# Kernel tuning notes

Measured on AMD Instinct MI355X. Metric: run time of the kernel, lower is better.

## Reference

```python
import jax, jax.numpy as jnp
import numpy as np

GC_ALPHA = 3.0  # saturation factor in MTGNN-style graph constructor
TOP_K = 5       # ctor arg: GraphConstructor(n_classes, 5, dim)
EPS_NORM = 1e-12


def setup_inputs() -> dict:
    key = jax.random.key(0)
    k1, k2, k3, k4, k5 = jax.random.split(key, 5)
    B, C, H, W = 32, 384, 80, 80
    N = 27
    return {
        "x": jax.random.normal(k1, (B, C, H, W), dtype=jnp.float32),
        "alpha": jnp.ones((), dtype=jnp.float32),
        "clusters": jax.random.normal(k2, (N, C), dtype=jnp.float32),
        "gc_w1": jax.random.normal(k3, (C, C), dtype=jnp.float32) / np.sqrt(C),
        "gc_w2": jax.random.normal(k4, (C, C), dtype=jnp.float32) / np.sqrt(C),
        "gcn_w": jax.random.normal(k5, (C, C), dtype=jnp.float32) / np.sqrt(C),
    }


def _refine_clusters(clusters, gc_w1, gc_w2, gcn_w):
    # GraphConstructor: learned asymmetric adjacency over n_classes nodes, top-k sparsified
    n = clusters.shape[0]
    a = jnp.tanh(GC_ALPHA * (clusters @ gc_w1))          # [n, d]
    b = jnp.tanh(GC_ALPHA * (clusters @ gc_w2))          # [n, d]
    adj = jax.nn.relu(jnp.tanh(GC_ALPHA * (a @ b.T - b @ a.T)))  # [n, n]
    topv, _ = jax.lax.top_k(adj, TOP_K)
    A = jnp.where(adj >= topv[:, -1:], adj, 0.0)         # keep top-k per row
    # GCNConv (no bias): add self-loops, symmetric normalization
    A_hat = A + jnp.eye(n, dtype=A.dtype)
    dinv = 1.0 / jnp.sqrt(A_hat.sum(axis=1))
    A_norm = dinv[:, None] * A_hat * dinv[None, :]
    return A_norm @ (clusters @ gcn_w)                   # [n, d]


def reference(x, alpha, clusters, gc_w1, gc_w2, gcn_w):
    # mp=True path: refine codebook with tiny GCN over learned graph
    cl = _refine_clusters(clusters, gc_w1, gc_w2, gcn_w)
    # cosine similarity of per-pixel features against codebook
    nc = cl / jnp.maximum(jnp.linalg.norm(cl, axis=1, keepdims=True), EPS_NORM)
    nf = x / jnp.maximum(jnp.linalg.norm(x, axis=1, keepdims=True), EPS_NORM)
    inner_products = jnp.einsum('bchw,nc->bnhw', nf, nc)          # [B, n, H, W]
    cluster_probs = jax.nn.softmax(inner_products * alpha, axis=1)
    cluster_loss = -(cluster_probs * inner_products).sum(axis=1).mean()
    # entropy over unnormalized similarities (computed in original forward)
    p = jax.nn.softmax(jnp.einsum('bchw,nc->bnhw', x, clusters), axis=1)
    entropy = (-(p * jnp.log(p + 1e-10)).sum(axis=1)).mean()
    return cluster_loss, inner_products, cl, entropy
```

## Files before the change

### kernel.cpp

```cpp
#include <hip/hip_runtime.h>
#include <math.h>

#define N_CL   27
#define C_DIM  384
#define HW_SZ  6400
#define B_SZ   32
#define NPIX   (B_SZ*HW_SZ)
#define NTILE  3200
#define NCHUNK 12
#define WSF_PARTS 24576
#define WSF_ADJ   40000
#define ENT_OFF (1 + (size_t)NPIX*N_CL + (size_t)N_CL*C_DIM)

typedef unsigned short ushort_t;
using bf16x8 = __attribute__((ext_vector_type(8))) short;
using f32x4  = __attribute__((ext_vector_type(4))) float;

__device__ __forceinline__ float xla_tanh_f32(float x) {
    const float c = 7.99881172180175781f;
    if (fabsf(x) < 0.0004f) return x;
    const float xc = fminf(fmaxf(x, -c), c);
    const float x2 = xc*xc;
    float p = fmaf(x2, -2.76076847742355e-16f, 2.00018790482477e-13f);
    p = fmaf(x2, p, -8.60467152213735e-11f);
    p = fmaf(x2, p,  5.12229709037114e-08f);
    p = fmaf(x2, p,  1.48572235717979e-05f);
    p = fmaf(x2, p,  6.37261928875436e-04f);
    p = fmaf(x2, p,  4.89352455891786e-03f);
    p = xc*p;
    float q = fmaf(x2, 1.19825839466702e-06f, 1.18534705686654e-04f);
    q = fmaf(x2, q, 2.26843463243900e-03f);
    q = fmaf(x2, q, 4.89352518554385e-03f);
    return p/q;
}

__global__ __launch_bounds__(384) void cl_refine_mm(const float* __restrict__ clusters,
                                                    const float* __restrict__ w1,
                                                    const float* __restrict__ w2,
                                                    const float* __restrict__ w3,
                                                    float* __restrict__ ws) {
    const int i = blockIdx.x;
    const int m = blockIdx.y;
    const int j = threadIdx.x;
    __shared__ float crow[C_DIM];
    crow[j] = clusters[i*C_DIM + j];
    __syncthreads();
    const float* __restrict__ W = (m==0) ? w1 : (m==1) ? w2 : w3;
    float s0=0.f,s1=0.f,s2=0.f,s3=0.f;
    #pragma unroll 4
    for (int k=0;k<C_DIM;k+=4){
        s0 = fmaf(crow[k+0], W[(size_t)(k+0)*C_DIM + j], s0);
        s1 = fmaf(crow[k+1], W[(size_t)(k+1)*C_DIM + j], s1);
        s2 = fmaf(crow[k+2], W[(size_t)(k+2)*C_DIM + j], s2);
        s3 = fmaf(crow[k+3], W[(size_t)(k+3)*C_DIM + j], s3);
    }
    const float acc = (s0+s1)+(s2+s3);
    ws[(size_t)m*N_CL*C_DIM + i*C_DIM + j] = (m<2) ? xla_tanh_f32(3.0f*acc) : acc;
}

__global__ __launch_bounds__(64) void cl_adj(const float* __restrict__ ws,
                                             float* __restrict__ adj_out) {
    const float* __restrict__ Am = ws;
    const float* __restrict__ Bm = ws + N_CL*C_DIM;
    const int i = blockIdx.x / N_CL, j = blockIdx.x - (blockIdx.x / N_CL)*N_CL;
    const int lane = threadIdx.x;
    float p=0.f, q=0.f;
    #pragma unroll
    for (int e=0;e<6;e++){
        const int k = e*64 + lane;
        p = fmaf(Am[i*C_DIM+k], Bm[j*C_DIM+k], p);
        q = fmaf(Bm[i*C_DIM+k], Am[j*C_DIM+k], q);
    }
    float d = p - q;
    #pragma unroll
    for (int m=1;m<64;m<<=1) d += __shfl_xor(d, m);
    if (lane==0) adj_out[blockIdx.x] = fmaxf(xla_tanh_f32(3.0f*d), 0.f);
}

__global__ __launch_bounds__(1024) void cl_graph2(float* ws,
                                                  const float* __restrict__ clusters_g,
                                                  float* __restrict__ out) {
    const float* cg = ws + 2*N_CL*C_DIM;
    float* cl_out = out + 1 + (size_t)NPIX*N_CL;
    const int t = threadIdx.x;

    __shared__ float anorm[N_CL][N_CL+1];
    __shared__ float dinv[N_CL];
    __shared__ float rinv[N_CL];
    __shared__ float cls[N_CL][C_DIM];

    if (t < N_CL*N_CL) {
        const int i = t / N_CL, j = t - (t / N_CL)*N_CL;
        anorm[i][j] = ws[WSF_ADJ + t];
    }
    __syncthreads();
    if (t < N_CL) {
        unsigned mask=0; float thr=0.f;
        for (int s=0;s<5;s++){
            float bv=-1.f; int bi2=0;
            for (int j=0;j<N_CL;j++){
                if (mask & (1u<<j)) continue;
                const float v = anorm[t][j];
                if (v > bv){ bv=v; bi2=j; }
            }
            mask |= 1u<<bi2; thr = bv;
        }
        float rs=0.f;
        for (int j=0;j<N_CL;j++){
            float v = anorm[t][j];
            v = (v >= thr) ? v : 0.f;
            if (j==t) v += 1.f;
            anorm[t][j] = v;
            rs += v;
        }
        dinv[t] = 1.0f / sqrtf(rs);
    }
    __syncthreads();
    if (t < N_CL*N_CL) {
        const int i = t / N_CL, j = t - (t / N_CL)*N_CL;
        anorm[i][j] = dinv[i]*anorm[i][j]*dinv[j];
    }
    __syncthreads();
    for (int idx=t; idx<N_CL*C_DIM; idx+=1024){
        const int i = idx / C_DIM, d = idx - i*C_DIM;
        float s=0.f;
        #pragma unroll
        for (int j=0;j<N_CL;j++) s = fmaf(anorm[i][j], cg[(size_t)j*C_DIM + d], s);
        cls[i][d] = s;
        cl_out[idx] = s;
    }
    __syncthreads();
    if (t < N_CL) {
        float ssq=0.f;
        for (int d=0; d<C_DIM; d++){ const float v=cls[t][d]; ssq=fmaf(v,v,ssq); }
        rinv[t] = 1.0f / fmaxf(sqrtf(ssq), 1e-12f);
    }
    __syncthreads();
    ushort_t* wpk = (ushort_t*)ws;
    for (int idx=t; idx<64*C_DIM; idx+=1024){
        const int n = idx / C_DIM, k = idx - n*C_DIM;
        float v = 0.f;
        if (n < N_CL) v = cls[n][k] * rinv[n];
        else if (n >= 32 && n < 32+N_CL) v = clusters_g[(size_t)(n-32)*C_DIM + k];
        const unsigned bits = __float_as_uint(v);
        const ushort_t hi = (ushort_t)(bits >> 16);
        const float lof = v - __uint_as_float(bits & 0xFFFF0000u);
        const ushort_t lo = (ushort_t)(__float_as_uint(lof) >> 16);
        wpk[idx] = hi;
        wpk[64*C_DIM + idx] = lo;
    }
}

__global__ __launch_bounds__(256, 6) void cl_mfma(const float* __restrict__ x,
                                                  const float* __restrict__ alpha_p,
                                                  const ushort_t* __restrict__ wpk,
                                                  float* __restrict__ ws,
                                                  float* __restrict__ out) {
    __shared__ __align__(16) ushort_t lB[2][2][64][40];
    __shared__ float redL[4], redE[4];

    const int tid = threadIdx.x;
    const int blk = blockIdx.x;
    const int b   = blk / 100;
    const int hw0 = (blk - b*100) * 64;
    const float* __restrict__ xb = x + (size_t)b*C_DIM*HW_SZ + hw0;

    const int lane = tid & 63;
    const int w    = tid >> 6;
    const int l15  = lane & 15;
    const int g    = lane >> 4;
    const int k0   = g*8;
    const int apx  = w*16 + l15;
    const float* __restrict__ xl = xb + apx;

    const int b_n  = tid >> 2;
    const int b_kb = (tid & 3) * 8;

    uint4 rb0, rb1;
    #define LOADB(c) {                                                            \
        rb0 = *(const uint4*)(wpk + (size_t)(     b_n)*C_DIM + (c)*32 + b_kb);    \
        rb1 = *(const uint4*)(wpk + (size_t)(64 + b_n)*C_DIM + (c)*32 + b_kb); }
    #define WRITEB(bf) {                                                          \
        *(uint4*)(&lB[bf][0][b_n][b_kb]) = rb0;                                   \
        *(uint4*)(&lB[bf][1][b_n][b_kb]) = rb1; }

    #define LOADA(c, R0,R1,R2,R3,R4,R5,R6,R7) {                                   \
        const float* pA = xl + (size_t)((c)*32 + k0)*HW_SZ;                       \
        R0 = pA[0*HW_SZ]; R1 = pA[1*HW_SZ]; R2 = pA[2*HW_SZ]; R3 = pA[3*HW_SZ];  \
        R4 = pA[4*HW_SZ]; R5 = pA[5*HW_SZ]; R6 = pA[6*HW_SZ]; R7 = pA[7*HW_SZ]; }

    union { ushort_t u[8]; bf16x8 v; } Ah;
    float ss = 0.f;
    #define CVT1(e, R) {                                                          \
        Ah.u[e] = (ushort_t)(__float_as_uint(R) >> 16);                           \
        ss = fmaf(R, R, ss); }
    #define CONVERT(R0,R1,R2,R3,R4,R5,R6,R7) {                                    \
        CVT1(0,R0) CVT1(1,R1) CVT1(2,R2) CVT1(3,R3)                               \
        CVT1(4,R4) CVT1(5,R5) CVT1(6,R6) CVT1(7,R7) }

    f32x4 acc0={0,0,0,0}, acc1={0,0,0,0}, acc2={0,0,0,0}, acc3={0,0,0,0};
    #define DOMFMA(cur) {                                                         \
        _Pragma("unroll")                                                         \
        for (int t = 0; t < 4; t++) {                                             \
            union { uint4 q; bf16x8 v; } Bh, Bl;                                  \
            Bh.q = *(const uint4*)(&lB[cur][0][t*16 + l15][k0]);                  \
            Bl.q = *(const uint4*)(&lB[cur][1][t*16 + l15][k0]);                  \
            f32x4 a = (t==0)?acc0:(t==1)?acc1:(t==2)?acc2:acc3;                   \
            a = __builtin_amdgcn_mfma_f32_16x16x32_bf16(Ah.v, Bh.v, a, 0,0,0);    \
            a = __builtin_amdgcn_mfma_f32_16x16x32_bf16(Ah.v, Bl.v, a, 0,0,0);    \
            if (t==0) acc0=a; else if (t==1) acc1=a; else if (t==2) acc2=a;       \
            else acc3=a;                                                          \
        } }

    #define KBAR() { asm volatile("s_waitcnt lgkmcnt(0)" ::: "memory");           \
                     __builtin_amdgcn_s_barrier(); }

    float Ra0,Ra1,Ra2,Ra3,Ra4,Ra5,Ra6,Ra7;
    float Rb0,Rb1,Rb2,Rb3,Rb4,Rb5,Rb6,Rb7;

    LOADB(0); WRITEB(0);
    LOADB(1);
    LOADA(0, Ra0,Ra1,Ra2,Ra3,Ra4,Ra5,Ra6,Ra7);
    LOADA(1, Rb0,Rb1,Rb2,Rb3,Rb4,Rb5,Rb6,Rb7);
    KBAR();

    for (int cc = 0; cc < NCHUNK; cc += 2) {
        CONVERT(Ra0,Ra1,Ra2,Ra3,Ra4,Ra5,Ra6,Ra7);
        DOMFMA(0);
        if (cc + 1 < NCHUNK) WRITEB(1);
        if (cc + 2 < NCHUNK) {
            LOADB(cc+2);
            LOADA(cc+2, Ra0,Ra1,Ra2,Ra3,Ra4,Ra5,Ra6,Ra7);
        }
        if (cc + 1 < NCHUNK) KBAR();
        CONVERT(Rb0,Rb1,Rb2,Rb3,Rb4,Rb5,Rb6,Rb7);
        DOMFMA(1);
        if (cc + 2 < NCHUNK) WRITEB(0);
        if (cc + 3 < NCHUNK) {
            LOADB(cc+3);
            LOADA(cc+3, Rb0,Rb1,Rb2,Rb3,Rb4,Rb5,Rb6,Rb7);
        }
        if (cc + 2 < NCHUNK) KBAR();
    }

    ss += __shfl_xor(ss, 16);
    ss += __shfl_xor(ss, 32);
    f32x4 invv;
    #pragma unroll
    for (int r = 0; r < 4; r++) {
        const float s2 = __shfl(ss, g*4 + r);
        invv[r] = 1.0f / fmaxf(sqrtf(s2), 1e-12f);
    }

    const float alpha = alpha_p[0];
    float* __restrict__ out1 = out + 1;
    const int pxb = hw0 + w*16 + g*4;

    f32x4 st0, st1;
    #pragma unroll
    for (int r=0;r<4;r++){ st0[r] = acc0[r]*invv[r]; st1[r] = acc1[r]*invv[r]; }
    *(f32x4*)(out1 + (size_t)b*N_CL*HW_SZ + (size_t)l15*HW_SZ + pxb) = st0;
    if (l15 <= 10)
        *(f32x4*)(out1 + (size_t)b*N_CL*HW_SZ + (size_t)(16+l15)*HW_SZ + pxb) = st1;

    float wloss = 0.f, went = 0.f;
    #pragma unroll
    for (int r=0;r<4;r++){
        const float ip0 = st0[r], ip1 = st1[r];
        const float v0 = alpha*ip0;
        const float v1 = (l15<=10) ? alpha*ip1 : -INFINITY;
        float mx = fmaxf(v0, v1);
        #pragma unroll
        for (int m=1;m<16;m<<=1) mx = fmaxf(mx, __shfl_xor(mx, m));
        const float e0 = expf(v0 - mx);
        const float e1 = (l15<=10) ? expf(v1 - mx) : 0.f;
        float z = e0 + e1;
        float tt = fmaf(e0, ip0, (l15<=10) ? e1*ip1 : 0.f);
        #pragma unroll
        for (int m=1;m<16;m<<=1){ z += __shfl_xor(z,m); tt += __shfl_xor(tt,m); }
        wloss += tt/z;
        const float c0 = acc2[r];
        const float c1 = (l15<=10) ? acc3[r] : -INFINITY;
        float emx = fmaxf(c0, c1);
        #pragma unroll
        for (int m=1;m<16;m<<=1) emx = fmaxf(emx, __shfl_xor(emx, m));
        const float f0 = expf(c0 - emx);
        const float f1 = (l15<=10) ? expf(c1 - emx) : 0.f;
        float ez = f0 + f1;
        #pragma unroll
        for (int m=1;m<16;m<<=1) ez += __shfl_xor(ez,m);
        const float iz = 1.0f/ez;
        const float p0 = f0*iz, p1 = f1*iz;
        float te = -p0*logf(p0+1e-10f) - p1*logf(p1+1e-10f);
        #pragma unroll
        for (int m=1;m<16;m<<=1) te += __shfl_xor(te,m);
        went += te;
    }
    wloss += __shfl_xor(wloss,16); wloss += __shfl_xor(wloss,32);
    went  += __shfl_xor(went ,16); went  += __shfl_xor(went ,32);
    if (lane == 0) { redL[w] = wloss; redE[w] = went; }
    __syncthreads();
    if (tid == 0) {
        float* parts = ws + WSF_PARTS;
        parts[blk]         = redL[0]+redL[1]+redL[2]+redL[3];
        parts[NTILE + blk] = redE[0]+redE[1]+redE[2]+redE[3];
    }
}

__global__ __launch_bounds__(1024) void cl_final_reduce(const float* __restrict__ ws,
                                                        float* __restrict__ out) {
    __shared__ float r[1024];
    const int t = threadIdx.x;
    const float* parts = ws + WSF_PARTS;
    float s = 0.f;
    for (int j=t; j<NTILE; j+=1024) s += parts[j];
    r[t] = s; __syncthreads();
    for (int sft=512;sft>0;sft>>=1){ if (t<sft) r[t]+=r[t+sft]; __syncthreads(); }
    if (t==0) out[0] = -r[0]*(1.0f/NPIX);
    __syncthreads();
    s = 0.f;
    for (int j=t; j<NTILE; j+=1024) s += parts[NTILE + j];
    r[t] = s; __syncthreads();
    for (int sft=512;sft>0;sft>>=1){ if (t<sft) r[t]+=r[t+sft]; __syncthreads(); }
    if (t==0) out[ENT_OFF] = r[0]*(1.0f/NPIX);
}

extern "C" void kernel_launch(void* const* d_in, const int* in_sizes, int n_in,
                              void* d_out, int out_size, void* d_ws, size_t ws_size,
                              hipStream_t stream) {
    const float* x        = (const float*)d_in[0];
    const float* alpha    = (const float*)d_in[1];
    const float* clusters = (const float*)d_in[2];
    const float* w1       = (const float*)d_in[3];
    const float* w2       = (const float*)d_in[4];
    const float* w3       = (const float*)d_in[5];
    float* out = (float*)d_out;
    float* ws  = (float*)d_ws;

    cl_refine_mm<<<dim3(27,3), dim3(384), 0, stream>>>(clusters, w1, w2, w3, ws);
    cl_adj<<<dim3(N_CL*N_CL), dim3(64), 0, stream>>>(ws, ws + WSF_ADJ);
    cl_graph2<<<dim3(1), dim3(1024), 0, stream>>>(ws, clusters, out);
    cl_mfma<<<dim3(NTILE), dim3(256), 0, stream>>>(x, alpha, (const ushort_t*)ws, ws, out);
    cl_final_reduce<<<dim3(1), dim3(1024), 0, stream>>>(ws, out);
}
```

Baseline: 140.3 us.

## Fuse adjacency into graph kernel and final reduce into main kernel via ticket

```diff
diff --git a/kernel.cpp b/kernel.cpp
--- a/kernel.cpp
+++ b/kernel.cpp
@@ -9,7 +9,7 @@
 #define NTILE  3200
 #define NCHUNK 12
 #define WSF_PARTS 24576
-#define WSF_ADJ   40000
+#define WSF_CNT   31104
 #define ENT_OFF (1 + (size_t)NPIX*N_CL + (size_t)N_CL*C_DIM)
 
 typedef unsigned short ushort_t;
@@ -58,40 +58,37 @@
     ws[(size_t)m*N_CL*C_DIM + i*C_DIM + j] = (m<2) ? xla_tanh_f32(3.0f*acc) : acc;
 }
 
-__global__ __launch_bounds__(64) void cl_adj(const float* __restrict__ ws,
-                                             float* __restrict__ adj_out) {
-    const float* __restrict__ Am = ws;
-    const float* __restrict__ Bm = ws + N_CL*C_DIM;
-    const int i = blockIdx.x / N_CL, j = blockIdx.x - (blockIdx.x / N_CL)*N_CL;
-    const int lane = threadIdx.x;
-    float p=0.f, q=0.f;
-    #pragma unroll
-    for (int e=0;e<6;e++){
-        const int k = e*64 + lane;
-        p = fmaf(Am[i*C_DIM+k], Bm[j*C_DIM+k], p);
-        q = fmaf(Bm[i*C_DIM+k], Am[j*C_DIM+k], q);
-    }
-    float d = p - q;
-    #pragma unroll
-    for (int m=1;m<64;m<<=1) d += __shfl_xor(d, m);
-    if (lane==0) adj_out[blockIdx.x] = fmaxf(xla_tanh_f32(3.0f*d), 0.f);
-}
-
-__global__ __launch_bounds__(1024) void cl_graph2(float* ws,
-                                                  const float* __restrict__ clusters_g,
-                                                  float* __restrict__ out) {
+__global__ __launch_bounds__(1024) void cl_adj_graph(float* ws,
+                                                     const float* __restrict__ clusters_g,
+                                                     float* __restrict__ out) {
     const float* cg = ws + 2*N_CL*C_DIM;
     float* cl_out = out + 1 + (size_t)NPIX*N_CL;
     const int t = threadIdx.x;
 
+    __shared__ float Ash[N_CL][C_DIM+1];
+    __shared__ float Bsh[N_CL][C_DIM+1];
     __shared__ float anorm[N_CL][N_CL+1];
     __shared__ float dinv[N_CL];
     __shared__ float rinv[N_CL];
     __shared__ float cls[N_CL][C_DIM];
 
+    for (int idx=t; idx<N_CL*C_DIM; idx+=1024){
+        const int i = idx / C_DIM, k = idx - i*C_DIM;
+        Ash[i][k] = ws[idx];
+        Bsh[i][k] = ws[N_CL*C_DIM + idx];
+    }
+    __syncthreads();
     if (t < N_CL*N_CL) {
         const int i = t / N_CL, j = t - (t / N_CL)*N_CL;
-        anorm[i][j] = ws[WSF_ADJ + t];
+        float p0=0,p1=0,p2=0,p3=0,q0=0,q1=0,q2=0,q3=0;
+        for (int k=0;k<C_DIM;k+=4){
+            p0=fmaf(Ash[i][k+0],Bsh[j][k+0],p0); p1=fmaf(Ash[i][k+1],Bsh[j][k+1],p1);
+            p2=fmaf(Ash[i][k+2],Bsh[j][k+2],p2); p3=fmaf(Ash[i][k+3],Bsh[j][k+3],p3);
+            q0=fmaf(Bsh[i][k+0],Ash[j][k+0],q0); q1=fmaf(Bsh[i][k+1],Ash[j][k+1],q1);
+            q2=fmaf(Bsh[i][k+2],Ash[j][k+2],q2); q3=fmaf(Bsh[i][k+3],Ash[j][k+3],q3);
+        }
+        const float s1v=(p0+p1)+(p2+p3), s2v=(q0+q1)+(q2+q3);
+        anorm[i][j] = fmaxf(xla_tanh_f32(3.0f*(s1v-s2v)), 0.f);
     }
     __syncthreads();
     if (t < N_CL) {
@@ -135,6 +132,7 @@
         for (int d=0; d<C_DIM; d++){ const float v=cls[t][d]; ssq=fmaf(v,v,ssq); }
         rinv[t] = 1.0f / fmaxf(sqrtf(ssq), 1e-12f);
     }
+    if (t == 0) *(unsigned*)(ws + WSF_CNT) = 0u;
     __syncthreads();
     ushort_t* wpk = (ushort_t*)ws;
     for (int idx=t; idx<64*C_DIM; idx+=1024){
@@ -158,6 +156,8 @@
                                                   float* __restrict__ out) {
     __shared__ __align__(16) ushort_t lB[2][2][64][40];
     __shared__ float redL[4], redE[4];
+    __shared__ float fin[256];
+    __shared__ unsigned ticket_s;
 
     const int tid = threadIdx.x;
     const int blk = blockIdx.x;
@@ -170,8 +170,7 @@
     const int l15  = lane & 15;
     const int g    = lane >> 4;
     const int k0   = g*8;
-    const int apx  = w*16 + l15;
-    const float* __restrict__ xl = xb + apx;
+    const float* __restrict__ xl = xb + (w*16 + l15);
 
     const int b_n  = tid >> 2;
     const int b_kb = (tid & 3) * 8;
@@ -300,29 +299,32 @@
     went  += __shfl_xor(went ,16); went  += __shfl_xor(went ,32);
     if (lane == 0) { redL[w] = wloss; redE[w] = went; }
     __syncthreads();
+
+    float* parts = ws + WSF_PARTS;
     if (tid == 0) {
-        float* parts = ws + WSF_PARTS;
-        parts[blk]         = redL[0]+redL[1]+redL[2]+redL[3];
-        parts[NTILE + blk] = redE[0]+redE[1]+redE[2]+redE[3];
-    }
-}
-
-__global__ __launch_bounds__(1024) void cl_final_reduce(const float* __restrict__ ws,
-                                                        float* __restrict__ out) {
-    __shared__ float r[1024];
-    const int t = threadIdx.x;
-    const float* parts = ws + WSF_PARTS;
-    float s = 0.f;
-    for (int j=t; j<NTILE; j+=1024) s += parts[j];
-    r[t] = s; __syncthreads();
-    for (int sft=512;sft>0;sft>>=1){ if (t<sft) r[t]+=r[t+sft]; __syncthreads(); }
-    if (t==0) out[0] = -r[0]*(1.0f/NPIX);
-    __syncthreads();
-    s = 0.f;
-    for (int j=t; j<NTILE; j+=1024) s += parts[NTILE + j];
-    r[t] = s; __syncthreads();
-    for (int sft=512;sft>0;sft>>=1){ if (t<sft) r[t]+=r[t+sft]; __syncthreads(); }
-    if (t==0) out[ENT_OFF] = r[0]*(1.0f/NPIX);
+        __hip_atomic_store(&parts[blk], redL[0]+redL[1]+redL[2]+redL[3],
+                           __ATOMIC_RELAXED, __HIP_MEMORY_SCOPE_AGENT);
+        __hip_atomic_store(&parts[NTILE + blk], redE[0]+redE[1]+redE[2]+redE[3],
+                           __ATOMIC_RELAXED, __HIP_MEMORY_SCOPE_AGENT);
+        ticket_s = __hip_atomic_fetch_add((unsigned*)(ws + WSF_CNT), 1u,
+                                          __ATOMIC_ACQ_REL, __HIP_MEMORY_SCOPE_AGENT);
+    }
+    __syncthreads();
+    if (ticket_s == NTILE - 1) {
+        float s = 0.f;
+        for (int j = tid; j < NTILE; j += 256)
+            s += __hip_atomic_load(&parts[j], __ATOMIC_RELAXED, __HIP_MEMORY_SCOPE_AGENT);
+        fin[tid] = s; __syncthreads();
+        for (int st=128; st>0; st>>=1){ if (tid<st) fin[tid]+=fin[tid+st]; __syncthreads(); }
+        if (tid == 0) out[0] = -fin[0]*(1.0f/NPIX);
+        __syncthreads();
+        s = 0.f;
+        for (int j = tid; j < NTILE; j += 256)
+            s += __hip_atomic_load(&parts[NTILE + j], __ATOMIC_RELAXED, __HIP_MEMORY_SCOPE_AGENT);
+        fin[tid] = s; __syncthreads();
+        for (int st=128; st>0; st>>=1){ if (tid<st) fin[tid]+=fin[tid+st]; __syncthreads(); }
+        if (tid == 0) out[ENT_OFF] = fin[0]*(1.0f/NPIX);
+    }
 }
 
 extern "C" void kernel_launch(void* const* d_in, const int* in_sizes, int n_in,
@@ -338,8 +340,6 @@
     float* ws  = (float*)d_ws;
 
     cl_refine_mm<<<dim3(27,3), dim3(384), 0, stream>>>(clusters, w1, w2, w3, ws);
-    cl_adj<<<dim3(N_CL*N_CL), dim3(64), 0, stream>>>(ws, ws + WSF_ADJ);
-    cl_graph2<<<dim3(1), dim3(1024), 0, stream>>>(ws, clusters, out);
+    cl_adj_graph<<<dim3(1), dim3(1024), 0, stream>>>(ws, clusters, out);
     cl_mfma<<<dim3(NTILE), dim3(256), 0, stream>>>(x, alpha, (const ushort_t*)ws, ws, out);
-    cl_final_reduce<<<dim3(1), dim3(1024), 0, stream>>>(ws, out);
-}
+}
```

Result: slower. 314.7 us (+124.2%).
